# Kernel tuning notes

Hardware: AMD Instinct MI355X
Metric: run time of the kernel (lower is better)

Reference implementation:

```python
import jax, jax.numpy as jnp
import numpy as np

N = 50000      # nodes
E = 600000     # edges
C = 128        # in_channels
H = 128        # hidden_channels
O = 128        # out_channels
G = 512        # graphs in batch
BN_EPS = 1e-5


def setup_inputs() -> dict:
    key = jax.random.key(0)
    ks = jax.random.split(key, 16)

    def w(k, shape):
        return jax.random.normal(k, shape, dtype=jnp.float32) * 0.05

    inp = {}
    inp["x"] = jax.random.normal(ks[0], (N, C), dtype=jnp.float32)
    inp["edge_index"] = jax.random.randint(ks[1], (2, E), 0, N, dtype=jnp.int64)
    inp["batch"] = jnp.sort(jax.random.randint(ks[2], (N,), 0, G, dtype=jnp.int64))

    dims = [(C, H, H), (H, H, H), (H, H, O)]
    ki = 3
    for li, (din, dh, dout) in enumerate(dims, 1):
        inp[f"g{li}_W1"] = w(ks[ki], (din, dh)); inp[f"g{li}_b1"] = jnp.zeros((dh,), jnp.float32)
        inp[f"g{li}_gm"] = jnp.ones((dh,), jnp.float32); inp[f"g{li}_bt"] = jnp.zeros((dh,), jnp.float32)
        inp[f"g{li}_rm"] = jnp.zeros((dh,), jnp.float32); inp[f"g{li}_rv"] = jnp.ones((dh,), jnp.float32)
        inp[f"g{li}_W2"] = w(ks[ki + 1], (dh, dout)); inp[f"g{li}_b2"] = jnp.zeros((dout,), jnp.float32)
        ki += 2
    inp["lin_W"] = w(ks[ki], (H + H + O, O))
    inp["lin_b"] = jnp.zeros((O,), jnp.float32)
    return inp


def gin_conv(x, src, dst, W1, b1, gm, bt, rm, rv, W2, b2):
    # GINConv (eps=0): mlp(x + sum_{j in N(i)} x_j); mlp = Linear-BN(eval)-ReLU-Linear
    agg = jax.ops.segment_sum(x[src], dst, num_segments=N)   # [N, d] scatter-add
    h = (x + agg) @ W1 + b1
    h = (h - rm) * jax.lax.rsqrt(rv + BN_EPS) * gm + bt      # BatchNorm1d, eval mode
    return jax.nn.relu(h) @ W2 + b2


def reference(x, edge_index, batch,
              g1_W1, g1_b1, g1_gm, g1_bt, g1_rm, g1_rv, g1_W2, g1_b2,
              g2_W1, g2_b1, g2_gm, g2_bt, g2_rm, g2_rv, g2_W2, g2_b2,
              g3_W1, g3_b1, g3_gm, g3_bt, g3_rm, g3_rv, g3_W2, g3_b2,
              lin_W, lin_b):
    src, dst = edge_index[0], edge_index[1]
    # dropout(0.2) is identity in eval mode
    x1 = jax.nn.relu(gin_conv(x, src, dst, g1_W1, g1_b1, g1_gm, g1_bt, g1_rm, g1_rv, g1_W2, g1_b2))
    x2 = jax.nn.relu(gin_conv(x1, src, dst, g2_W1, g2_b1, g2_gm, g2_bt, g2_rm, g2_rv, g2_W2, g2_b2))
    x3 = gin_conv(x2, src, dst, g3_W1, g3_b1, g3_gm, g3_bt, g3_rm, g3_rv, g3_W2, g3_b2)
    xc = jnp.concatenate([x1, x2, x3], axis=-1)              # JumpingKnowledge 'cat' -> [N, H+H+O]
    sums = jax.ops.segment_sum(xc, batch, num_segments=G)    # global_mean_pool
    cnt = jax.ops.segment_sum(jnp.ones((N, 1), xc.dtype), batch, num_segments=G)
    pooled = sums / jnp.maximum(cnt, 1.0)                    # [G, H+H+O]
    return pooled @ lin_W + lin_b                            # [G, O]
```

## Files before the change

kernel.cpp:

```cpp
#include <hip/hip_runtime.h>
#include <hip/hip_bf16.h>

#define NNODES 50000
#define NEDGES 600000
#define NGRAPHS 512
#define BN_EPS 1e-5f

typedef short bf16x8 __attribute__((ext_vector_type(8)));
typedef float f32x4 __attribute__((ext_vector_type(4)));

__device__ __forceinline__ void bf_split(float x, ushort& h, ushort& l) {
    __hip_bfloat16 bh = __float2bfloat16(x);
    float r = x - __bfloat162float(bh);
    __hip_bfloat16 bl = __float2bfloat16(r);
    h = __builtin_bit_cast(ushort, bh);
    l = __builtin_bit_cast(ushort, bl);
}
__device__ __forceinline__ ushort f2b(float x) {
    return __builtin_bit_cast(ushort, __float2bfloat16(x));
}
__device__ __forceinline__ float b2f(ushort u) {
    union { uint i; float f; } c; c.i = ((uint)u) << 16; return c.f;
}

__global__ __launch_bounds__(256) void prep_kernel(
    const float* __restrict__ x, ushort* __restrict__ xh,
    float* __restrict__ pooled, int* __restrict__ counts, int* __restrict__ row_ptr,
    const float* W0, const float* W1, const float* W2, const float* W3,
    const float* W4, const float* W5, ushort* __restrict__ hi, ushort* __restrict__ lo) {
    int b = blockIdx.x, t = threadIdx.x;
    if (b < 3125) {
        int f4 = b * 512 + t * 2;
        float4 a0 = ((const float4*)x)[f4];
        float4 a1 = ((const float4*)x)[f4 + 1];
        ushort4 u0 = {f2b(a0.x), f2b(a0.y), f2b(a0.z), f2b(a0.w)};
        ushort4 u1 = {f2b(a1.x), f2b(a1.y), f2b(a1.z), f2b(a1.w)};
        int e0 = f4 * 4;
        *(ushort4*)(xh + e0) = u0;
        *(ushort4*)(xh + e0 + 4) = u1;
        if (b == 0 && t == 0) row_ptr[NNODES] = NEDGES;
    } else if (b < 3317) {
        ((float4*)pooled)[(b - 3125) * 256 + t] = make_float4(0.f, 0.f, 0.f, 0.f);
    } else if (b < 3513) {
        int i = (b - 3317) * 256 + t;
        if (i < NNODES) counts[i] = 0;
    } else {
        int wb = b - 3513;
        const float* Ws[6] = {W0, W1, W2, W3, W4, W5};
        const float* W = Ws[wb >> 4];
        ushort* h = hi + (size_t)(wb >> 4) * 16384;
        ushort* l = lo + (size_t)(wb >> 4) * 16384;
        int chunk = wb & 15;
#pragma unroll
        for (int i = 0; i < 4; i++) {
            int idx = chunk * 1024 + i * 256 + t;
            int n = idx >> 7, k = idx & 127;
            ushort hh, ll;
            bf_split(W[k * 128 + n], hh, ll);
            h[n * 128 + k] = hh;
            l[n * 128 + k] = ll;
        }
    }
}

__global__ __launch_bounds__(256) void hist_kernel(const int* __restrict__ dst,
                                                   int* __restrict__ counts, int E) {
    int i = blockIdx.x * 256 + threadIdx.x;
    if (i < E) atomicAdd(&counts[dst[i]], 1);
}

__global__ __launch_bounds__(256) void scan1_kernel(const int* __restrict__ counts,
                                                    int* __restrict__ partials, int n) {
    __shared__ int s[256];
    int i = blockIdx.x * 256 + threadIdx.x;
    int v = (i < n) ? counts[i] : 0;
    s[threadIdx.x] = v;
    __syncthreads();
    for (int off = 128; off > 0; off >>= 1) {
        if (threadIdx.x < off) s[threadIdx.x] += s[threadIdx.x + off];
        __syncthreads();
    }
    if (threadIdx.x == 0) partials[blockIdx.x] = s[0];
}

__global__ __launch_bounds__(256) void scan3_kernel(const int* __restrict__ counts,
                                                    const int* __restrict__ partials,
                                                    int* __restrict__ row_ptr,
                                                    int* __restrict__ cursor, int n, int nb) {
    __shared__ int s[256];
    __shared__ int base_sh;
    int t = threadIdx.x;
    int pv = (t < (int)blockIdx.x && t < nb) ? partials[t] : 0;
    s[t] = pv;
    __syncthreads();
    for (int off = 128; off > 0; off >>= 1) {
        if (t < off) s[t] += s[t + off];
        __syncthreads();
    }
    if (t == 0) base_sh = s[0];
    __syncthreads();
    int base = base_sh;
    int i = blockIdx.x * 256 + t;
    int v = (i < n) ? counts[i] : 0;
    __syncthreads();
    s[t] = v;
    __syncthreads();
    for (int off = 1; off < 256; off <<= 1) {
        int nv = (t >= off) ? s[t - off] : 0;
        __syncthreads();
        s[t] += nv;
        __syncthreads();
    }
    if (i < n) {
        int ex = base + s[t] - v;
        row_ptr[i] = ex;
        cursor[i] = ex;
    }
}

__global__ __launch_bounds__(256) void scatter_kernel(const int* __restrict__ src,
                                                      const int* __restrict__ dst,
                                                      int* __restrict__ cursor,
                                                      int* __restrict__ esrc, int E) {
    int i = blockIdx.x * 256 + threadIdx.x;
    if (i < E) {
        int p = atomicAdd(&cursor[dst[i]], 1);
        esrc[p] = src[i];
    }
}

template <bool SELF_F32>
__global__ __launch_bounds__(256) void agg_kernel(
    const float* __restrict__ xf,
    const ushort* __restrict__ phi, const ushort* __restrict__ plo,
    const int* __restrict__ rp, const int* __restrict__ esrc,
    ushort* __restrict__ ohi, ushort* __restrict__ olo, int n) {
    int wid  = (blockIdx.x * 256 + threadIdx.x) >> 6;
    int lane = threadIdx.x & 63;
    int node = wid * 2 + (lane >> 5);
    int q = lane & 31;
    if (node >= n) return;
    const ushort4* xh = (const ushort4*)phi;
    float4 acc;
    if (SELF_F32) {
        acc = ((const float4*)xf)[(size_t)node * 32 + q];
    } else {
        ushort4 sh = xh[(size_t)node * 32 + q];
        ushort4 sl = ((const ushort4*)plo)[(size_t)node * 32 + q];
        acc.x = b2f(sh.x) + b2f(sl.x);
        acc.y = b2f(sh.y) + b2f(sl.y);
        acc.z = b2f(sh.z) + b2f(sl.z);
        acc.w = b2f(sh.w) + b2f(sl.w);
    }
    int beg = rp[node], end = rp[node + 1];
    int e = beg;
    for (; e + 8 <= end; e += 8) {
        int i0 = esrc[e],     i1 = esrc[e + 1], i2 = esrc[e + 2], i3 = esrc[e + 3];
        int i4 = esrc[e + 4], i5 = esrc[e + 5], i6 = esrc[e + 6], i7 = esrc[e + 7];
        ushort4 v0 = xh[(size_t)i0 * 32 + q];
        ushort4 v1 = xh[(size_t)i1 * 32 + q];
        ushort4 v2 = xh[(size_t)i2 * 32 + q];
        ushort4 v3 = xh[(size_t)i3 * 32 + q];
        ushort4 v4 = xh[(size_t)i4 * 32 + q];
        ushort4 v5 = xh[(size_t)i5 * 32 + q];
        ushort4 v6 = xh[(size_t)i6 * 32 + q];
        ushort4 v7 = xh[(size_t)i7 * 32 + q];
        acc.x += ((b2f(v0.x) + b2f(v1.x)) + (b2f(v2.x) + b2f(v3.x))) +
                 ((b2f(v4.x) + b2f(v5.x)) + (b2f(v6.x) + b2f(v7.x)));
        acc.y += ((b2f(v0.y) + b2f(v1.y)) + (b2f(v2.y) + b2f(v3.y))) +
                 ((b2f(v4.y) + b2f(v5.y)) + (b2f(v6.y) + b2f(v7.y)));
        acc.z += ((b2f(v0.z) + b2f(v1.z)) + (b2f(v2.z) + b2f(v3.z))) +
                 ((b2f(v4.z) + b2f(v5.z)) + (b2f(v6.z) + b2f(v7.z)));
        acc.w += ((b2f(v0.w) + b2f(v1.w)) + (b2f(v2.w) + b2f(v3.w))) +
                 ((b2f(v4.w) + b2f(v5.w)) + (b2f(v6.w) + b2f(v7.w)));
    }
    for (; e + 2 <= end; e += 2) {
        int i0 = esrc[e], i1 = esrc[e + 1];
        ushort4 v0 = xh[(size_t)i0 * 32 + q];
        ushort4 v1 = xh[(size_t)i1 * 32 + q];
        acc.x += b2f(v0.x) + b2f(v1.x); acc.y += b2f(v0.y) + b2f(v1.y);
        acc.z += b2f(v0.z) + b2f(v1.z); acc.w += b2f(v0.w) + b2f(v1.w);
    }
    for (; e < end; e++) {
        ushort4 v = xh[(size_t)esrc[e] * 32 + q];
        acc.x += b2f(v.x); acc.y += b2f(v.y); acc.z += b2f(v.z); acc.w += b2f(v.w);
    }
    ushort4 hh, ll;
    bf_split(acc.x, hh.x, ll.x);
    bf_split(acc.y, hh.y, ll.y);
    bf_split(acc.z, hh.z, ll.z);
    bf_split(acc.w, hh.w, ll.w);
    *(ushort4*)(ohi + (size_t)node * 128 + q * 4) = hh;
    *(ushort4*)(olo + (size_t)node * 128 + q * 4) = ll;
}

#define HP 136
template <bool RELU_OUT>
__global__ __launch_bounds__(256) void mlp_kernel(
    const ushort* __restrict__ Ahi, const ushort* __restrict__ Alo,
    const ushort* __restrict__ W1hi, const ushort* __restrict__ W1lo,
    const ushort* __restrict__ W2hi, const ushort* __restrict__ W2lo,
    const float* __restrict__ b1, const float* __restrict__ gm,
    const float* __restrict__ bt, const float* __restrict__ rm,
    const float* __restrict__ rv, const float* __restrict__ b2,
    ushort* __restrict__ Chi, ushort* __restrict__ Clo, int M) {
    __shared__ __align__(16) ushort smem[2 * 128 * HP];
#define AS(b_, p_, o_) smem[(((b_) * 2 + (p_)) << 12) + (o_)]
#define HS(p_, o_) smem[(p_)*128 * HP + (o_)]
    const int t = threadIdx.x;
    const int lane = t & 63;
    const int wv = t >> 6;
    const int wr = wv >> 1, wc = wv & 1;
    const int row0 = blockIdx.x * 128;
    const int g = lane >> 4, c = lane & 15;

    const int m0 = t >> 2,  k80 = (t & 3) * 8;
    const int m1 = m0 + 64;
    int r0 = row0 + m0; if (r0 >= M) r0 = M - 1;
    int r1 = row0 + m1; if (r1 >= M) r1 = M - 1;
    const size_t ga0 = (size_t)r0 * 128 + k80;
    const size_t ga1 = (size_t)r1 * 128 + k80;
    const int la0 = m0 * 32 + k80, la1 = m1 * 32 + k80;

    f32x4 acc[4][4];
#pragma unroll
    for (int i = 0; i < 4; i++)
#pragma unroll
        for (int j = 0; j < 4; j++) acc[i][j] = (f32x4){0.f, 0.f, 0.f, 0.f};

    uint4 ph0 = *(const uint4*)(Ahi + ga0);
    uint4 ph1 = *(const uint4*)(Ahi + ga1);
    uint4 pl0 = *(const uint4*)(Alo + ga0);
    uint4 pl1 = *(const uint4*)(Alo + ga1);
    *(uint4*)&AS(0, 0, la0) = ph0;
    *(uint4*)&AS(0, 0, la1) = ph1;
    *(uint4*)&AS(0, 1, la0) = pl0;
    *(uint4*)&AS(0, 1, la1) = pl1;
    __syncthreads();

    int cur = 0;
    for (int kb = 0; kb < 4; kb++) {
        bf16x8 bh[4], bl[4];
#pragma unroll
        for (int ct = 0; ct < 4; ct++) {
            const size_t wo = (size_t)(wc * 64 + ct * 16 + c) * 128 + kb * 32 + g * 8;
            bh[ct] = *(const bf16x8*)(W1hi + wo);
            bl[ct] = *(const bf16x8*)(W1lo + wo);
        }
        if (kb < 3) {
            const size_t o = (size_t)(kb + 1) * 32;
            ph0 = *(const uint4*)(Ahi + ga0 + o);
            ph1 = *(const uint4*)(Ahi + ga1 + o);
            pl0 = *(const uint4*)(Alo + ga0 + o);
            pl1 = *(const uint4*)(Alo + ga1 + o);
        }
        bf16x8 ah[4], al[4];
#pragma unroll
        for (int rt = 0; rt < 4; rt++) {
            int off = (wr * 64 + rt * 16 + c) * 32 + g * 8;
            ah[rt] = *(bf16x8*)&AS(cur, 0, off);
            al[rt] = *(bf16x8*)&AS(cur, 1, off);
        }
#pragma unroll
        for (int rt = 0; rt < 4; rt++)
#pragma unroll
            for (int ct = 0; ct < 4; ct++) {
                acc[rt][ct] = __builtin_amdgcn_mfma_f32_16x16x32_bf16(ah[rt], bh[ct], acc[rt][ct], 0, 0, 0);
                acc[rt][ct] = __builtin_amdgcn_mfma_f32_16x16x32_bf16(ah[rt], bl[ct], acc[rt][ct], 0, 0, 0);
                acc[rt][ct] = __builtin_amdgcn_mfma_f32_16x16x32_bf16(al[rt], bh[ct], acc[rt][ct], 0, 0, 0);
            }
        if (kb < 3) {
            *(uint4*)&AS(cur ^ 1, 0, la0) = ph0;
            *(uint4*)&AS(cur ^ 1, 0, la1) = ph1;
            *(uint4*)&AS(cur ^ 1, 1, la0) = pl0;
            *(uint4*)&AS(cur ^ 1, 1, la1) = pl1;
        }
        __syncthreads();
        cur ^= 1;
    }

    {
        float cs[4], ca[4];
#pragma unroll
        for (int ct = 0; ct < 4; ct++) {
            int n = wc * 64 + ct * 16 + c;
            float s = gm[n] * rsqrtf(rv[n] + BN_EPS);
            cs[ct] = s;
            ca[ct] = (b1[n] - rm[n]) * s + bt[n];
        }
#pragma unroll
        for (int rt = 0; rt < 4; rt++)
#pragma unroll
            for (int r = 0; r < 4; r++) {
                int row = wr * 64 + rt * 16 + g * 4 + r;
#pragma unroll
                for (int ct = 0; ct < 4; ct++) {
                    int col = wc * 64 + ct * 16 + c;
                    float v = fmaxf(acc[rt][ct][r] * cs[ct] + ca[ct], 0.f);
                    ushort hh, ll;
                    bf_split(v, hh, ll);
                    HS(0, row * HP + col) = hh;
                    HS(1, row * HP + col) = ll;
                }
            }
    }
    __syncthreads();

#pragma unroll
    for (int i = 0; i < 4; i++)
#pragma unroll
        for (int j = 0; j < 4; j++) acc[i][j] = (f32x4){0.f, 0.f, 0.f, 0.f};

    for (int kb = 0; kb < 4; kb++) {
        bf16x8 bh[4], bl[4];
#pragma unroll
        for (int ct = 0; ct < 4; ct++) {
            const size_t wo = (size_t)(wc * 64 + ct * 16 + c) * 128 + kb * 32 + g * 8;
            bh[ct] = *(const bf16x8*)(W2hi + wo);
            bl[ct] = *(const bf16x8*)(W2lo + wo);
        }
        bf16x8 ah[4], al[4];
#pragma unroll
        for (int rt = 0; rt < 4; rt++) {
            int off = (wr * 64 + rt * 16 + c) * HP + kb * 32 + g * 8;
            ah[rt] = *(bf16x8*)&HS(0, off);
            al[rt] = *(bf16x8*)&HS(1, off);
        }
#pragma unroll
        for (int rt = 0; rt < 4; rt++)
#pragma unroll
            for (int ct = 0; ct < 4; ct++) {
                acc[rt][ct] = __builtin_amdgcn_mfma_f32_16x16x32_bf16(ah[rt], bh[ct], acc[rt][ct], 0, 0, 0);
                acc[rt][ct] = __builtin_amdgcn_mfma_f32_16x16x32_bf16(ah[rt], bl[ct], acc[rt][ct], 0, 0, 0);
                acc[rt][ct] = __builtin_amdgcn_mfma_f32_16x16x32_bf16(al[rt], bh[ct], acc[rt][ct], 0, 0, 0);
            }
    }

    float ca2[4];
#pragma unroll
    for (int ct = 0; ct < 4; ct++) ca2[ct] = b2[wc * 64 + ct * 16 + c];
#pragma unroll
    for (int rt = 0; rt < 4; rt++)
#pragma unroll
        for (int r = 0; r < 4; r++) {
            int row = row0 + wr * 64 + rt * 16 + g * 4 + r;
            if (row < M) {
#pragma unroll
                for (int ct = 0; ct < 4; ct++) {
                    int col = wc * 64 + ct * 16 + c;
                    float v = acc[rt][ct][r] + ca2[ct];
                    if (RELU_OUT) v = fmaxf(v, 0.f);
                    ushort hh, ll;
                    bf_split(v, hh, ll);
                    Chi[(size_t)row * 128 + col] = hh;
                    Clo[(size_t)row * 128 + col] = ll;
                }
            }
        }
#undef AS
#undef HS
}

__global__ __launch_bounds__(384) void pool_kernel(
    const ushort* __restrict__ x1h, const ushort* __restrict__ x1l,
    const ushort* __restrict__ x2h, const ushort* __restrict__ x2l,
    const ushort* __restrict__ x3h, const ushort* __restrict__ x3l,
    const int* __restrict__ batch, float* __restrict__ pooled, int n) {
    __shared__ int bs[32];
    int b0 = blockIdx.x * 32;
    int t = threadIdx.x;
    int rows = n - b0; if (rows > 32) rows = 32;
    if (t < rows) bs[t] = batch[b0 + t];
    __syncthreads();
    const ushort* ph = (t < 128) ? x1h : ((t < 256) ? x2h : x3h);
    const ushort* pl = (t < 128) ? x1l : ((t < 256) ? x2l : x3l);
    int ch = t & 127;
    int gcur = bs[0];
    float acc = 0.f;
#pragma unroll 8
    for (int r = 0; r < rows; r++) {
        int gg = bs[r];
        if (gg != gcur) {
            atomicAdd(&pooled[gcur * 384 + t], acc);
            acc = 0.f;
            gcur = gg;
        }
        size_t o = (size_t)(b0 + r) * 128 + ch;
        acc += b2f(ph[o]) + b2f(pl[o]);
    }
    atomicAdd(&pooled[gcur * 384 + t], acc);
}

__global__ __launch_bounds__(128) void final_kernel(const float* __restrict__ pooled,
                                                    const int* __restrict__ batch,
                                                    const float* __restrict__ W,
                                                    const float* __restrict__ b,
                                                    float* __restrict__ out, int n) {
    __shared__ float ps[384];
    int gph = blockIdx.x, t = threadIdx.x;
    int lo1 = 0, hi1 = n;
    while (lo1 < hi1) { int mid = (lo1 + hi1) >> 1; if (batch[mid] < gph) lo1 = mid + 1; else hi1 = mid; }
    int start = lo1;
    int lo2 = start, hi2 = n;
    while (lo2 < hi2) { int mid = (lo2 + hi2) >> 1; if (batch[mid] < gph + 1) lo2 = mid + 1; else hi2 = mid; }
    int cnt = lo2 - start;
    float inv = 1.f / (float)(cnt > 0 ? cnt : 1);
    for (int i = t; i < 384; i += 128) ps[i] = pooled[gph * 384 + i] * inv;
    __syncthreads();
    float acc = b[t];
#pragma unroll 8
    for (int k = 0; k < 384; k++) acc += ps[k] * W[k * 128 + t];
    out[gph * 128 + t] = acc;
}

extern "C" void kernel_launch(void* const* d_in, const int* in_sizes, int n_in,
                              void* d_out, int out_size, void* d_ws, size_t ws_size,
                              hipStream_t stream) {
    const float* x     = (const float*)d_in[0];
    const int*   edge  = (const int*)d_in[1];
    const int*   batch = (const int*)d_in[2];
    const float* p[32];
    for (int i = 0; i < n_in && i < 32; i++) p[i] = (const float*)d_in[i];
    const float* lin_W = p[27];
    const float* lin_b = p[28];

    char* w = (char*)d_ws;
    auto alloc = [&](size_t bytes) { void* r = (void*)w; w += (bytes + 255) & ~(size_t)255; return r; };
    const size_t PL = (size_t)NNODES * 128;
    ushort* thi   = (ushort*)alloc(PL * 2);
    ushort* tlo   = (ushort*)alloc(PL * 2);
    ushort* xh0   = (ushort*)alloc(PL * 2);
    ushort* p1h   = (ushort*)alloc(PL * 2);
    ushort* p1l   = (ushort*)alloc(PL * 2);
    ushort* p2h   = xh0;
    ushort* p2l   = (ushort*)alloc(PL * 2);
    ushort* p3h   = (ushort*)alloc(PL * 2);
    ushort* p3l   = (ushort*)alloc(PL * 2);
    float* pooled = (float*)alloc((size_t)NGRAPHS * 384 * 4);
    int* counts   = (int*)alloc((size_t)NNODES * 4);
    int* cursor   = (int*)alloc((size_t)NNODES * 4);
    int* row_ptr  = (int*)alloc((size_t)(NNODES + 1) * 4);
    int* esrc     = (int*)alloc((size_t)NEDGES * 4);
    int* partials = (int*)alloc(256 * 4);
    ushort* wt_hi = (ushort*)alloc((size_t)6 * 16384 * 2);
    ushort* wt_lo = (ushort*)alloc((size_t)6 * 16384 * 2);

    const int* src = edge;
    const int* dst = edge + NEDGES;

    prep_kernel<<<3609, 256, 0, stream>>>(x, xh0, pooled, counts, row_ptr,
                                          p[3], p[9], p[11], p[17], p[19], p[25],
                                          wt_hi, wt_lo);

    int nb = (NNODES + 255) / 256;
    hist_kernel<<<(NEDGES + 255) / 256, 256, 0, stream>>>(dst, counts, NEDGES);
    scan1_kernel<<<nb, 256, 0, stream>>>(counts, partials, NNODES);
    scan3_kernel<<<nb, 256, 0, stream>>>(counts, partials, row_ptr, cursor, NNODES, nb);
    scatter_kernel<<<(NEDGES + 255) / 256, 256, 0, stream>>>(src, dst, cursor, esrc, NEDGES);

    int mlp_grid = (NNODES + 127) / 128;
    int agg_grid = (NNODES / 2 * 64 + 255) / 256;

    agg_kernel<true><<<agg_grid, 256, 0, stream>>>(x, xh0, nullptr, row_ptr, esrc,
                                                   thi, tlo, NNODES);
    mlp_kernel<true><<<mlp_grid, 256, 0, stream>>>(thi, tlo,
        wt_hi + 0 * 16384, wt_lo + 0 * 16384, wt_hi + 1 * 16384, wt_lo + 1 * 16384,
        p[4], p[5], p[6], p[7], p[8], p[10], p1h, p1l, NNODES);
    agg_kernel<false><<<agg_grid, 256, 0, stream>>>(nullptr, p1h, p1l, row_ptr, esrc,
                                                    thi, tlo, NNODES);
    mlp_kernel<true><<<mlp_grid, 256, 0, stream>>>(thi, tlo,
        wt_hi + 2 * 16384, wt_lo + 2 * 16384, wt_hi + 3 * 16384, wt_lo + 3 * 16384,
        p[12], p[13], p[14], p[15], p[16], p[18], p2h, p2l, NNODES);
    agg_kernel<false><<<agg_grid, 256, 0, stream>>>(nullptr, p2h, p2l, row_ptr, esrc,
                                                    thi, tlo, NNODES);
    mlp_kernel<false><<<mlp_grid, 256, 0, stream>>>(thi, tlo,
        wt_hi + 4 * 16384, wt_lo + 4 * 16384, wt_hi + 5 * 16384, wt_lo + 5 * 16384,
        p[20], p[21], p[22], p[23], p[24], p[26], p3h, p3l, NNODES);

    pool_kernel<<<(NNODES + 31) / 32, 384, 0, stream>>>(p1h, p1l, p2h, p2l, p3h, p3l,
                                                        batch, pooled, NNODES);
    final_kernel<<<NGRAPHS, 128, 0, stream>>>(pooled, batch, lin_W, lin_b,
                                              (float*)d_out, NNODES);
}
```

Measured before the change: 403.2 us.

## Fuse global mean pooling into MLP epilogue and halve MLP row tile

Global mean pooling now runs inside each MLP kernel's epilogue. Outputs are staged in shared memory and summed per graph segment with atomics, which removes the separate pool kernel. The third layer no longer writes its hi/lo bf16 output planes to global memory, since only the pooled sums are needed. The MLP row tile is also cut from 128 to 64 rows, doubling the grid and shrinking LDS and register use. The cost is extra atomics and a shared-memory reduction in every MLP block, plus less weight reuse per block.

```diff
diff --git a/kernel.cpp b/kernel.cpp
--- a/kernel.cpp
+++ b/kernel.cpp
@@ -194,8 +194,7 @@
     *(ushort4*)(olo + (size_t)node * 128 + q * 4) = ll;
 }
 
-#define HP 136
-template <bool RELU_OUT>
+template <bool RELU_OUT, bool WRITE_PLANES>
 __global__ __launch_bounds__(256) void mlp_kernel(
     const ushort* __restrict__ Ahi, const ushort* __restrict__ Alo,
     const ushort* __restrict__ W1hi, const ushort* __restrict__ W1lo,
@@ -203,39 +202,36 @@
     const float* __restrict__ b1, const float* __restrict__ gm,
     const float* __restrict__ bt, const float* __restrict__ rm,
     const float* __restrict__ rv, const float* __restrict__ b2,
-    ushort* __restrict__ Chi, ushort* __restrict__ Clo, int M) {
-    __shared__ __align__(16) ushort smem[2 * 128 * HP];
-#define AS(b_, p_, o_) smem[(((b_) * 2 + (p_)) << 12) + (o_)]
-#define HS(p_, o_) smem[(p_)*128 * HP + (o_)]
+    ushort* __restrict__ Chi, ushort* __restrict__ Clo,
+    const int* __restrict__ batch, float* __restrict__ pooled, int poff, int M) {
+    __shared__ __align__(16) ushort smem[2 * 64 * 136];
+    __shared__ int bsm[64];
+#define AS(b_, p_, o_) smem[(((b_) * 2 + (p_)) << 11) + (o_)]
+#define HS(p_, o_) smem[(p_)*8704 + (o_)]
     const int t = threadIdx.x;
     const int lane = t & 63;
     const int wv = t >> 6;
     const int wr = wv >> 1, wc = wv & 1;
-    const int row0 = blockIdx.x * 128;
+    const int row0 = blockIdx.x * 64;
     const int g = lane >> 4, c = lane & 15;
 
-    const int m0 = t >> 2,  k80 = (t & 3) * 8;
-    const int m1 = m0 + 64;
+    if (t < 64) bsm[t] = (row0 + t < M) ? batch[row0 + t] : -1;
+
+    const int m0 = t >> 2, k80 = (t & 3) * 8;
     int r0 = row0 + m0; if (r0 >= M) r0 = M - 1;
-    int r1 = row0 + m1; if (r1 >= M) r1 = M - 1;
     const size_t ga0 = (size_t)r0 * 128 + k80;
-    const size_t ga1 = (size_t)r1 * 128 + k80;
-    const int la0 = m0 * 32 + k80, la1 = m1 * 32 + k80;
-
-    f32x4 acc[4][4];
-#pragma unroll
-    for (int i = 0; i < 4; i++)
+    const int la0 = m0 * 32 + k80;
+
+    f32x4 acc[2][4];
+#pragma unroll
+    for (int i = 0; i < 2; i++)
 #pragma unroll
         for (int j = 0; j < 4; j++) acc[i][j] = (f32x4){0.f, 0.f, 0.f, 0.f};
 
     uint4 ph0 = *(const uint4*)(Ahi + ga0);
-    uint4 ph1 = *(const uint4*)(Ahi + ga1);
     uint4 pl0 = *(const uint4*)(Alo + ga0);
-    uint4 pl1 = *(const uint4*)(Alo + ga1);
     *(uint4*)&AS(0, 0, la0) = ph0;
-    *(uint4*)&AS(0, 0, la1) = ph1;
     *(uint4*)&AS(0, 1, la0) = pl0;
-    *(uint4*)&AS(0, 1, la1) = pl1;
     __syncthreads();
 
     int cur = 0;
@@ -250,19 +246,17 @@
         if (kb < 3) {
             const size_t o = (size_t)(kb + 1) * 32;
             ph0 = *(const uint4*)(Ahi + ga0 + o);
-            ph1 = *(const uint4*)(Ahi + ga1 + o);
             pl0 = *(const uint4*)(Alo + ga0 + o);
-            pl1 = *(const uint4*)(Alo + ga1 + o);
-        }
-        bf16x8 ah[4], al[4];
-#pragma unroll
-        for (int rt = 0; rt < 4; rt++) {
-            int off = (wr * 64 + rt * 16 + c) * 32 + g * 8;
+        }
+        bf16x8 ah[2], al[2];
+#pragma unroll
+        for (int rt = 0; rt < 2; rt++) {
+            int off = (wr * 32 + rt * 16 + c) * 32 + g * 8;
             ah[rt] = *(bf16x8*)&AS(cur, 0, off);
             al[rt] = *(bf16x8*)&AS(cur, 1, off);
         }
 #pragma unroll
-        for (int rt = 0; rt < 4; rt++)
+        for (int rt = 0; rt < 2; rt++)
 #pragma unroll
             for (int ct = 0; ct < 4; ct++) {
                 acc[rt][ct] = __builtin_amdgcn_mfma_f32_16x16x32_bf16(ah[rt], bh[ct], acc[rt][ct], 0, 0, 0);
@@ -271,46 +265,39 @@
             }
         if (kb < 3) {
             *(uint4*)&AS(cur ^ 1, 0, la0) = ph0;
-            *(uint4*)&AS(cur ^ 1, 0, la1) = ph1;
             *(uint4*)&AS(cur ^ 1, 1, la0) = pl0;
-            *(uint4*)&AS(cur ^ 1, 1, la1) = pl1;
         }
         __syncthreads();
         cur ^= 1;
     }
 
     {
-        float cs[4], ca[4];
 #pragma unroll
         for (int ct = 0; ct < 4; ct++) {
             int n = wc * 64 + ct * 16 + c;
             float s = gm[n] * rsqrtf(rv[n] + BN_EPS);
-            cs[ct] = s;
-            ca[ct] = (b1[n] - rm[n]) * s + bt[n];
-        }
-#pragma unroll
-        for (int rt = 0; rt < 4; rt++)
-#pragma unroll
-            for (int r = 0; r < 4; r++) {
-                int row = wr * 64 + rt * 16 + g * 4 + r;
-#pragma unroll
-                for (int ct = 0; ct < 4; ct++) {
-                    int col = wc * 64 + ct * 16 + c;
-                    float v = fmaxf(acc[rt][ct][r] * cs[ct] + ca[ct], 0.f);
+            float ca = (b1[n] - rm[n]) * s + bt[n];
+#pragma unroll
+            for (int rt = 0; rt < 2; rt++)
+#pragma unroll
+                for (int r = 0; r < 4; r++) {
+                    int row = wr * 32 + rt * 16 + g * 4 + r;
+                    float v = fmaxf(acc[rt][ct][r] * s + ca, 0.f);
                     ushort hh, ll;
                     bf_split(v, hh, ll);
-                    HS(0, row * HP + col) = hh;
-                    HS(1, row * HP + col) = ll;
+                    HS(0, row * 136 + n) = hh;
+                    HS(1, row * 136 + n) = ll;
                 }
-            }
-    }
-    __syncthreads();
-
-#pragma unroll
-    for (int i = 0; i < 4; i++)
+        }
+    }
+    __syncthreads();
+
+#pragma unroll
+    for (int i = 0; i < 2; i++)
 #pragma unroll
         for (int j = 0; j < 4; j++) acc[i][j] = (f32x4){0.f, 0.f, 0.f, 0.f};
 
+#pragma unroll
     for (int kb = 0; kb < 4; kb++) {
         bf16x8 bh[4], bl[4];
 #pragma unroll
@@ -319,15 +306,15 @@
             bh[ct] = *(const bf16x8*)(W2hi + wo);
             bl[ct] = *(const bf16x8*)(W2lo + wo);
         }
-        bf16x8 ah[4], al[4];
-#pragma unroll
-        for (int rt = 0; rt < 4; rt++) {
-            int off = (wr * 64 + rt * 16 + c) * HP + kb * 32 + g * 8;
+        bf16x8 ah[2], al[2];
+#pragma unroll
+        for (int rt = 0; rt < 2; rt++) {
+            int off = (wr * 32 + rt * 16 + c) * 136 + kb * 32 + g * 8;
             ah[rt] = *(bf16x8*)&HS(0, off);
             al[rt] = *(bf16x8*)&HS(1, off);
         }
 #pragma unroll
-        for (int rt = 0; rt < 4; rt++)
+        for (int rt = 0; rt < 2; rt++)
 #pragma unroll
             for (int ct = 0; ct < 4; ct++) {
                 acc[rt][ct] = __builtin_amdgcn_mfma_f32_16x16x32_bf16(ah[rt], bh[ct], acc[rt][ct], 0, 0, 0);
@@ -335,60 +322,56 @@
                 acc[rt][ct] = __builtin_amdgcn_mfma_f32_16x16x32_bf16(al[rt], bh[ct], acc[rt][ct], 0, 0, 0);
             }
     }
-
-    float ca2[4];
-#pragma unroll
-    for (int ct = 0; ct < 4; ct++) ca2[ct] = b2[wc * 64 + ct * 16 + c];
-#pragma unroll
-    for (int rt = 0; rt < 4; rt++)
-#pragma unroll
-        for (int r = 0; r < 4; r++) {
-            int row = row0 + wr * 64 + rt * 16 + g * 4 + r;
-            if (row < M) {
+    __syncthreads();
+
+    float* P = (float*)smem;
+    {
+        float ca2[4];
+#pragma unroll
+        for (int ct = 0; ct < 4; ct++) ca2[ct] = b2[wc * 64 + ct * 16 + c];
+#pragma unroll
+        for (int rt = 0; rt < 2; rt++)
+#pragma unroll
+            for (int r = 0; r < 4; r++) {
+                int rl = wr * 32 + rt * 16 + g * 4 + r;
+                int row = row0 + rl;
+                bool valid = row < M;
 #pragma unroll
                 for (int ct = 0; ct < 4; ct++) {
                     int col = wc * 64 + ct * 16 + c;
                     float v = acc[rt][ct][r] + ca2[ct];
                     if (RELU_OUT) v = fmaxf(v, 0.f);
-                    ushort hh, ll;
-                    bf_split(v, hh, ll);
-                    Chi[(size_t)row * 128 + col] = hh;
-                    Clo[(size_t)row * 128 + col] = ll;
+                    P[rl * 132 + col] = valid ? v : 0.f;
+                    if (WRITE_PLANES && valid) {
+                        ushort hh, ll;
+                        bf_split(v, hh, ll);
+                        Chi[(size_t)row * 128 + col] = hh;
+                        Clo[(size_t)row * 128 + col] = ll;
+                    }
                 }
             }
-        }
+    }
+    __syncthreads();
+
+    {
+        int col = t & 127;
+        int rbase = (t >> 7) * 32;
+        int gcur = bsm[rbase];
+        float accp = 0.f;
+#pragma unroll 8
+        for (int r = 0; r < 32; r++) {
+            int gg = bsm[rbase + r];
+            if (gg != gcur) {
+                if (gcur >= 0) atomicAdd(&pooled[gcur * 384 + poff + col], accp);
+                accp = 0.f;
+                gcur = gg;
+            }
+            accp += P[(rbase + r) * 132 + col];
+        }
+        if (gcur >= 0) atomicAdd(&pooled[gcur * 384 + poff + col], accp);
+    }
 #undef AS
 #undef HS
-}
-
-__global__ __launch_bounds__(384) void pool_kernel(
-    const ushort* __restrict__ x1h, const ushort* __restrict__ x1l,
-    const ushort* __restrict__ x2h, const ushort* __restrict__ x2l,
-    const ushort* __restrict__ x3h, const ushort* __restrict__ x3l,
-    const int* __restrict__ batch, float* __restrict__ pooled, int n) {
-    __shared__ int bs[32];
-    int b0 = blockIdx.x * 32;
-    int t = threadIdx.x;
-    int rows = n - b0; if (rows > 32) rows = 32;
-    if (t < rows) bs[t] = batch[b0 + t];
-    __syncthreads();
-    const ushort* ph = (t < 128) ? x1h : ((t < 256) ? x2h : x3h);
-    const ushort* pl = (t < 128) ? x1l : ((t < 256) ? x2l : x3l);
-    int ch = t & 127;
-    int gcur = bs[0];
-    float acc = 0.f;
-#pragma unroll 8
-    for (int r = 0; r < rows; r++) {
-        int gg = bs[r];
-        if (gg != gcur) {
-            atomicAdd(&pooled[gcur * 384 + t], acc);
-            acc = 0.f;
-            gcur = gg;
-        }
-        size_t o = (size_t)(b0 + r) * 128 + ch;
-        acc += b2f(ph[o]) + b2f(pl[o]);
-    }
-    atomicAdd(&pooled[gcur * 384 + t], acc);
 }
 
 __global__ __launch_bounds__(128) void final_kernel(const float* __restrict__ pooled,
@@ -434,8 +417,6 @@
     ushort* p1l   = (ushort*)alloc(PL * 2);
     ushort* p2h   = xh0;
     ushort* p2l   = (ushort*)alloc(PL * 2);
-    ushort* p3h   = (ushort*)alloc(PL * 2);
-    ushort* p3l   = (ushort*)alloc(PL * 2);
     float* pooled = (float*)alloc((size_t)NGRAPHS * 384 * 4);
     int* counts   = (int*)alloc((size_t)NNODES * 4);
     int* cursor   = (int*)alloc((size_t)NNODES * 4);
@@ -458,27 +439,25 @@
     scan3_kernel<<<nb, 256, 0, stream>>>(counts, partials, row_ptr, cursor, NNODES, nb);
     scatter_kernel<<<(NEDGES + 255) / 256, 256, 0, stream>>>(src, dst, cursor, esrc, NEDGES);
 
-    int mlp_grid = (NNODES + 127) / 128;
+    int mlp_grid = (NNODES + 63) / 64;
     int agg_grid = (NNODES / 2 * 64 + 255) / 256;
 
     agg_kernel<true><<<agg_grid, 256, 0, stream>>>(x, xh0, nullptr, row_ptr, esrc,
                                                    thi, tlo, NNODES);
-    mlp_kernel<true><<<mlp_grid, 256, 0, stream>>>(thi, tlo,
+    mlp_kernel<true, true><<<mlp_grid, 256, 0, stream>>>(thi, tlo,
         wt_hi + 0 * 16384, wt_lo + 0 * 16384, wt_hi + 1 * 16384, wt_lo + 1 * 16384,
-        p[4], p[5], p[6], p[7], p[8], p[10], p1h, p1l, NNODES);
+        p[4], p[5], p[6], p[7], p[8], p[10], p1h, p1l, batch, pooled, 0, NNODES);
     agg_kernel<false><<<agg_grid, 256, 0, stream>>>(nullptr, p1h, p1l, row_ptr, esrc,
                                                     thi, tlo, NNODES);
-    mlp_kernel<true><<<mlp_grid, 256, 0, stream>>>(thi, tlo,
+    mlp_kernel<true, true><<<mlp_grid, 256, 0, stream>>>(thi, tlo,
         wt_hi + 2 * 16384, wt_lo + 2 * 16384, wt_hi + 3 * 16384, wt_lo + 3 * 16384,
-        p[12], p[13], p[14], p[15], p[16], p[18], p2h, p2l, NNODES);
+        p[12], p[13], p[14], p[15], p[16], p[18], p2h, p2l, batch, pooled, 128, NNODES);
     agg_kernel<false><<<agg_grid, 256, 0, stream>>>(nullptr, p2h, p2l, row_ptr, esrc,
                                                     thi, tlo, NNODES);
-    mlp_kernel<false><<<mlp_grid, 256, 0, stream>>>(thi, tlo,
+    mlp_kernel<false, false><<<mlp_grid, 256, 0, stream>>>(thi, tlo,
         wt_hi + 4 * 16384, wt_lo + 4 * 16384, wt_hi + 5 * 16384, wt_lo + 5 * 16384,
-        p[20], p[21], p[22], p[23], p[24], p[26], p3h, p3l, NNODES);
-
-    pool_kernel<<<(NNODES + 31) / 32, 384, 0, stream>>>(p1h, p1l, p2h, p2l, p3h, p3l,
-                                                        batch, pooled, NNODES);
+        p[20], p[21], p[22], p[23], p[24], p[26], nullptr, nullptr, batch, pooled, 256, NNODES);
+
     final_kernel<<<NGRAPHS, 128, 0, stream>>>(pooled, batch, lin_W, lin_b,
                                               (float*)d_out, NNODES);
 }
```

Result: slower. 413.3 us (+2.5%).

## Fuse global mean pooling into MLP epilogues and skip layer-3 plane writes

Applied to the files above, without the earlier changes.

Each MLP kernel now stages its fp32 output tile in shared memory and accumulates per-graph column sums into the pooled buffer with atomics, which removes the separate pool kernel. The last layer no longer writes its hi/lo bf16 output planes at all, since only the pooled sums consume them. This saves one launch and the re-read of three feature matrices. In exchange, every MLP kernel gets an extra shared-memory pass, two block barriers and atomics in its epilogue. Pooling now sums fp32 values directly rather than hi+lo bf16 pairs.

```diff
diff --git a/kernel.cpp b/kernel.cpp
--- a/kernel.cpp
+++ b/kernel.cpp
@@ -195,7 +195,7 @@
 }
 
 #define HP 136
-template <bool RELU_OUT>
+template <bool RELU_OUT, bool WRITE_PLANES>
 __global__ __launch_bounds__(256) void mlp_kernel(
     const ushort* __restrict__ Ahi, const ushort* __restrict__ Alo,
     const ushort* __restrict__ W1hi, const ushort* __restrict__ W1lo,
@@ -203,8 +203,10 @@
     const float* __restrict__ b1, const float* __restrict__ gm,
     const float* __restrict__ bt, const float* __restrict__ rm,
     const float* __restrict__ rv, const float* __restrict__ b2,
-    ushort* __restrict__ Chi, ushort* __restrict__ Clo, int M) {
+    ushort* __restrict__ Chi, ushort* __restrict__ Clo,
+    const int* __restrict__ batch, float* __restrict__ pooled, int poff, int M) {
     __shared__ __align__(16) ushort smem[2 * 128 * HP];
+    __shared__ int bsm[128];
 #define AS(b_, p_, o_) smem[(((b_) * 2 + (p_)) << 12) + (o_)]
 #define HS(p_, o_) smem[(p_)*128 * HP + (o_)]
     const int t = threadIdx.x;
@@ -213,6 +215,8 @@
     const int wr = wv >> 1, wc = wv & 1;
     const int row0 = blockIdx.x * 128;
     const int g = lane >> 4, c = lane & 15;
+
+    if (t < 128) bsm[t] = (row0 + t < M) ? batch[row0 + t] : -1;
 
     const int m0 = t >> 2,  k80 = (t & 3) * 8;
     const int m1 = m0 + 64;
@@ -335,60 +339,56 @@
                 acc[rt][ct] = __builtin_amdgcn_mfma_f32_16x16x32_bf16(al[rt], bh[ct], acc[rt][ct], 0, 0, 0);
             }
     }
-
-    float ca2[4];
-#pragma unroll
-    for (int ct = 0; ct < 4; ct++) ca2[ct] = b2[wc * 64 + ct * 16 + c];
-#pragma unroll
-    for (int rt = 0; rt < 4; rt++)
-#pragma unroll
-        for (int r = 0; r < 4; r++) {
-            int row = row0 + wr * 64 + rt * 16 + g * 4 + r;
-            if (row < M) {
+    __syncthreads();
+
+    float* P = (float*)smem;
+    {
+        float ca2[4];
+#pragma unroll
+        for (int ct = 0; ct < 4; ct++) ca2[ct] = b2[wc * 64 + ct * 16 + c];
+#pragma unroll
+        for (int rt = 0; rt < 4; rt++)
+#pragma unroll
+            for (int r = 0; r < 4; r++) {
+                int rl = wr * 64 + rt * 16 + g * 4 + r;
+                int row = row0 + rl;
+                bool valid = row < M;
 #pragma unroll
                 for (int ct = 0; ct < 4; ct++) {
                     int col = wc * 64 + ct * 16 + c;
                     float v = acc[rt][ct][r] + ca2[ct];
                     if (RELU_OUT) v = fmaxf(v, 0.f);
-                    ushort hh, ll;
-                    bf_split(v, hh, ll);
-                    Chi[(size_t)row * 128 + col] = hh;
-                    Clo[(size_t)row * 128 + col] = ll;
+                    P[rl * 132 + col] = valid ? v : 0.f;
+                    if (WRITE_PLANES && valid) {
+                        ushort hh, ll;
+                        bf_split(v, hh, ll);
+                        Chi[(size_t)row * 128 + col] = hh;
+                        Clo[(size_t)row * 128 + col] = ll;
+                    }
                 }
             }
-        }
+    }
+    __syncthreads();
+
+    {
+        int col = t & 127;
+        int rbase = (t >> 7) * 64;
+        int gcur = bsm[rbase];
+        float accp = 0.f;
+#pragma unroll 8
+        for (int r = 0; r < 64; r++) {
+            int gg = bsm[rbase + r];
+            if (gg != gcur) {
+                if (gcur >= 0) atomicAdd(&pooled[gcur * 384 + poff + col], accp);
+                accp = 0.f;
+                gcur = gg;
+            }
+            accp += P[(rbase + r) * 132 + col];
+        }
+        if (gcur >= 0) atomicAdd(&pooled[gcur * 384 + poff + col], accp);
+    }
 #undef AS
 #undef HS
-}
-
-__global__ __launch_bounds__(384) void pool_kernel(
-    const ushort* __restrict__ x1h, const ushort* __restrict__ x1l,
-    const ushort* __restrict__ x2h, const ushort* __restrict__ x2l,
-    const ushort* __restrict__ x3h, const ushort* __restrict__ x3l,
-    const int* __restrict__ batch, float* __restrict__ pooled, int n) {
-    __shared__ int bs[32];
-    int b0 = blockIdx.x * 32;
-    int t = threadIdx.x;
-    int rows = n - b0; if (rows > 32) rows = 32;
-    if (t < rows) bs[t] = batch[b0 + t];
-    __syncthreads();
-    const ushort* ph = (t < 128) ? x1h : ((t < 256) ? x2h : x3h);
-    const ushort* pl = (t < 128) ? x1l : ((t < 256) ? x2l : x3l);
-    int ch = t & 127;
-    int gcur = bs[0];
-    float acc = 0.f;
-#pragma unroll 8
-    for (int r = 0; r < rows; r++) {
-        int gg = bs[r];
-        if (gg != gcur) {
-            atomicAdd(&pooled[gcur * 384 + t], acc);
-            acc = 0.f;
-            gcur = gg;
-        }
-        size_t o = (size_t)(b0 + r) * 128 + ch;
-        acc += b2f(ph[o]) + b2f(pl[o]);
-    }
-    atomicAdd(&pooled[gcur * 384 + t], acc);
 }
 
 __global__ __launch_bounds__(128) void final_kernel(const float* __restrict__ pooled,
@@ -434,8 +434,6 @@
     ushort* p1l   = (ushort*)alloc(PL * 2);
     ushort* p2h   = xh0;
     ushort* p2l   = (ushort*)alloc(PL * 2);
-    ushort* p3h   = (ushort*)alloc(PL * 2);
-    ushort* p3l   = (ushort*)alloc(PL * 2);
     float* pooled = (float*)alloc((size_t)NGRAPHS * 384 * 4);
     int* counts   = (int*)alloc((size_t)NNODES * 4);
     int* cursor   = (int*)alloc((size_t)NNODES * 4);
@@ -463,22 +461,20 @@
 
     agg_kernel<true><<<agg_grid, 256, 0, stream>>>(x, xh0, nullptr, row_ptr, esrc,
                                                    thi, tlo, NNODES);
-    mlp_kernel<true><<<mlp_grid, 256, 0, stream>>>(thi, tlo,
+    mlp_kernel<true, true><<<mlp_grid, 256, 0, stream>>>(thi, tlo,
         wt_hi + 0 * 16384, wt_lo + 0 * 16384, wt_hi + 1 * 16384, wt_lo + 1 * 16384,
-        p[4], p[5], p[6], p[7], p[8], p[10], p1h, p1l, NNODES);
+        p[4], p[5], p[6], p[7], p[8], p[10], p1h, p1l, batch, pooled, 0, NNODES);
     agg_kernel<false><<<agg_grid, 256, 0, stream>>>(nullptr, p1h, p1l, row_ptr, esrc,
                                                     thi, tlo, NNODES);
-    mlp_kernel<true><<<mlp_grid, 256, 0, stream>>>(thi, tlo,
+    mlp_kernel<true, true><<<mlp_grid, 256, 0, stream>>>(thi, tlo,
         wt_hi + 2 * 16384, wt_lo + 2 * 16384, wt_hi + 3 * 16384, wt_lo + 3 * 16384,
-        p[12], p[13], p[14], p[15], p[16], p[18], p2h, p2l, NNODES);
+        p[12], p[13], p[14], p[15], p[16], p[18], p2h, p2l, batch, pooled, 128, NNODES);
     agg_kernel<false><<<agg_grid, 256, 0, stream>>>(nullptr, p2h, p2l, row_ptr, esrc,
                                                     thi, tlo, NNODES);
-    mlp_kernel<false><<<mlp_grid, 256, 0, stream>>>(thi, tlo,
+    mlp_kernel<false, false><<<mlp_grid, 256, 0, stream>>>(thi, tlo,
         wt_hi + 4 * 16384, wt_lo + 4 * 16384, wt_hi + 5 * 16384, wt_lo + 5 * 16384,
-        p[20], p[21], p[22], p[23], p[24], p[26], p3h, p3l, NNODES);
-
-    pool_kernel<<<(NNODES + 31) / 32, 384, 0, stream>>>(p1h, p1l, p2h, p2l, p3h, p3l,
-                                                        batch, pooled, NNODES);
+        p[20], p[21], p[22], p[23], p[24], p[26], nullptr, nullptr, batch, pooled, 256, NNODES);
+
     final_kernel<<<NGRAPHS, 128, 0, stream>>>(pooled, batch, lin_W, lin_b,
                                               (float*)d_out, NNODES);
 }
```

After: 381.0 us. 1.06x faster.
